# Kernel tuning notes

Hardware: AMD Instinct MI355X
Metric: run time of the kernel (lower is better)

## Reference

```python
import jax, jax.numpy as jnp
import numpy as np

DIM = 768
NUM_HEADS = 12
HEAD_DIM = DIM // NUM_HEADS
SCALE = HEAD_DIM ** -0.5


def setup_inputs() -> dict:
    key = jax.random.key(0)
    k1, k2, k3, k4 = jax.random.split(key, 4)
    B, N, C = 4, 2048, DIM
    x = jax.random.normal(k1, (B, N, C), dtype=jnp.float32)
    # nn.Linear(dim, 3*dim, bias=False): weight shape (3C, C), y = x @ W^T
    w_qkv = jax.random.normal(k2, (3 * C, C), dtype=jnp.float32) * (C ** -0.5)
    # nn.Linear(dim, dim) with default bias=True
    w_proj = jax.random.normal(k3, (C, C), dtype=jnp.float32) * (C ** -0.5)
    b_proj = jax.random.normal(k4, (C,), dtype=jnp.float32) * 0.02
    return {"x": x, "w_qkv": w_qkv, "w_proj": w_proj, "b_proj": b_proj}


def reference(x, w_qkv, w_proj, b_proj):
    B, N, C = x.shape
    H, D = NUM_HEADS, HEAD_DIM
    qkv = jnp.einsum('bnc,oc->bno', x, w_qkv)  # (B, N, 3C)
    qkv = qkv.reshape(B, N, 3, H, D).transpose(2, 0, 3, 1, 4)  # (3, B, H, N, D)
    q, k, v = qkv[0], qkv[1], qkv[2]
    attn = jnp.einsum('bhnd,bhmd->bhnm', q, k) * jnp.float32(SCALE)  # (B,H,N,N)
    attn = jax.nn.softmax(attn, axis=-1)
    out = jnp.einsum('bhnm,bhmd->bhnd', attn, v)  # (B,H,N,D)
    out = out.transpose(0, 2, 1, 3).reshape(B, N, C)
    out = jnp.einsum('bnc,oc->bno', out, w_proj) + b_proj
    return out
```

## Files before the change

kernel.cpp:

```cpp
#include <hip/hip_runtime.h>
#include <math.h>

#define B_ 4
#define N_ 2048
#define C_ 768
#define H_ 12
#define D_ 64
#define QKSCALE_ 0.18033688011112042f

typedef unsigned short u16;
typedef unsigned int u32;
typedef short s16x8 __attribute__((ext_vector_type(8)));
typedef float f32x4 __attribute__((ext_vector_type(4)));
typedef float f32x16 __attribute__((ext_vector_type(16)));

__device__ __forceinline__ u16 f2bf(float f) {
    union { float f; u32 u; } v; v.f = f;
    u32 r = (v.u + 0x7fffu + ((v.u >> 16) & 1u)) >> 16;
    return (u16)r;
}

__device__ __forceinline__ void gl_lds16(const u16* g, u16* l) {
    __builtin_amdgcn_global_load_lds(
        (__attribute__((address_space(1))) void*)g,
        (__attribute__((address_space(3))) void*)l, 16, 0, 0);
}

#define NX4_  (B_ * N_ * C_ / 4)
#define NWQ4_ (3 * C_ * C_ / 4)
#define NWP4_ (C_ * C_ / 4)
__global__ __launch_bounds__(256) void cvt_all(const float4* __restrict__ x,
                                               const float4* __restrict__ wq,
                                               const float4* __restrict__ wp,
                                               ushort4* __restrict__ xb,
                                               ushort4* __restrict__ wqb,
                                               ushort4* __restrict__ wpb)
{
    const int tot = NX4_ + NWQ4_ + NWP4_;
    int i = blockIdx.x * blockDim.x + threadIdx.x;
    const int stride = gridDim.x * blockDim.x;
    for (; i < tot; i += stride) {
        const float4* s; ushort4* d; int j;
        if (i < NX4_)              { s = x;  d = xb;  j = i; }
        else if (i < NX4_ + NWQ4_) { s = wq; d = wqb; j = i - NX4_; }
        else                       { s = wp; d = wpb; j = i - NX4_ - NWQ4_; }
        float4 v = s[j];
        ushort4 o;
        o.x = f2bf(v.x); o.y = f2bf(v.y); o.z = f2bf(v.z); o.w = f2bf(v.w);
        d[j] = o;
    }
}

template<int BM, int WPEU, bool OUT_BF16, bool BIAS, bool QSCALE>
__global__ __launch_bounds__(256, WPEU) void gemm_mfma(const u16* __restrict__ A,
                                                       const u16* __restrict__ Bm,
                                                       const float* __restrict__ bias,
                                                       void* __restrict__ Cout,
                                                       int M, int N, int K)
{
    constexpr int MF  = BM / 64;
    constexpr int AC  = BM / 32;
    constexpr int ASZ = BM * 64, BSZ = 128 * 64;
    __shared__ __align__(16) u16 As[2 * ASZ];
    __shared__ __align__(16) u16 Bs[2 * BSZ];
    const int tid  = threadIdx.x;
    const int wv   = tid >> 6;
    const int lane = tid & 63;
    const int l31  = lane & 31;
    const int hi   = lane >> 5;
    const int wm   = (wv >> 1) * (BM / 2);
    const int wn   = (wv & 1) * 64;

    const int gx   = gridDim.x;
    const int nwg  = gx * gridDim.y;
    const int wgid = blockIdx.y * gx + blockIdx.x;
    const int nid  = (wgid & 7) * (nwg >> 3) + (wgid >> 3);
    const int row0 = (nid / gx) * BM, col0 = (nid % gx) * 128;

    f32x16 acc[MF][2];
    #pragma unroll
    for (int i = 0; i < MF; i++)
        #pragma unroll
        for (int j = 0; j < 2; j++)
            #pragma unroll
            for (int r = 0; r < 16; r++) acc[i][j][r] = 0.f;

    const int srow   = lane >> 3;
    const int schunk = ((lane & 7) ^ srow) * 8;

    const int arow_base = (BM / 4) * wv;
    const u16* gA = A + (size_t)(row0 + arow_base + srow) * K + schunk;
    const u16* gB = Bm + (size_t)(col0 + 32 * wv + srow) * K + schunk;
    const int aoff = arow_base * 64;
    const int boff = (32 * wv) * 64;

    const int nIter = K / 64;

    #pragma unroll
    for (int c = 0; c < AC; c++)
        gl_lds16(gA + (size_t)(8 * c) * K, As + aoff + c * 8 * 64);
    #pragma unroll
    for (int c = 0; c < 4; c++)
        gl_lds16(gB + (size_t)(8 * c) * K, Bs + boff + c * 8 * 64);

    for (int t = 0; t < nIter; t++) {
        const int cur = t & 1;
        __syncthreads();
        if (t + 1 < nIter) {
            const int k1 = (t + 1) * 64;
            const int nb = cur ^ 1;
            #pragma unroll
            for (int c = 0; c < AC; c++)
                gl_lds16(gA + (size_t)(8 * c) * K + k1, As + nb * ASZ + aoff + c * 8 * 64);
            #pragma unroll
            for (int c = 0; c < 4; c++)
                gl_lds16(gB + (size_t)(8 * c) * K + k1, Bs + nb * BSZ + boff + c * 8 * 64);
        }
        const u16* __restrict__ Ac = As + cur * ASZ;
        const u16* __restrict__ Bc = Bs + cur * BSZ;
        #pragma unroll
        for (int kk = 0; kk < 4; kk++) {
            const int fo = ((2 * kk + hi) ^ (l31 & 7)) * 8;
            s16x8 af[MF], bfr[2];
            #pragma unroll
            for (int i = 0; i < MF; i++)
                af[i] = *(const s16x8*)&Ac[(wm + 32*i + l31) * 64 + fo];
            #pragma unroll
            for (int j = 0; j < 2; j++)
                bfr[j] = *(const s16x8*)&Bc[(wn + 32*j + l31) * 64 + fo];
            #pragma unroll
            for (int i = 0; i < MF; i++)
                #pragma unroll
                for (int j = 0; j < 2; j++)
                    acc[i][j] = __builtin_amdgcn_mfma_f32_32x32x16_bf16(af[i], bfr[j], acc[i][j], 0, 0, 0);
        }
    }

    #pragma unroll
    for (int i = 0; i < MF; i++) {
        #pragma unroll
        for (int j = 0; j < 2; j++) {
            const int col = col0 + wn + 32*j + l31;
            float bv = BIAS ? bias[col] : 0.f;
            #pragma unroll
            for (int r = 0; r < 16; r++) {
                const int row = row0 + wm + 32*i + (r & 3) + 8*(r >> 2) + 4*hi;
                float v = acc[i][j][r] + bv;
                if (QSCALE && col < C_) v *= QKSCALE_;
                if (OUT_BF16) ((u16*)Cout)[(size_t)row * N + col] = f2bf(v);
                else          ((float*)Cout)[(size_t)row * N + col] = v;
            }
        }
    }
}

__global__ __launch_bounds__(256, 3) void attn_mfma(const u16* __restrict__ qkv,
                                                    u16* __restrict__ attout)
{
    __shared__ __align__(16) u16 Ks[2][64 * 64];
    __shared__ __align__(16) u16 Vt[2][64][72];

    const int tid  = threadIdx.x;
    const int wv   = tid >> 6;
    const int lane = tid & 63;
    const int l31  = lane & 31;
    const int hi   = lane >> 5;

    const int wgid = blockIdx.y * gridDim.x + blockIdx.x;
    const int ix   = wgid >> 3;
    const int bh   = (wgid & 7) * 6 + (ix >> 4);
    const int n0   = (ix & 15) * 128;
    const int b = bh / H_, h = bh % H_;
    const size_t rs = 3 * C_;

    const u16* Qg = qkv + ((size_t)b * N_ + n0) * rs + h * D_;
    const u16* Kg = qkv + ((size_t)b * N_) * rs + C_ + h * D_;
    const u16* Vg = Kg + C_;

    s16x8 qf[4];
    #pragma unroll
    for (int kk = 0; kk < 4; kk++)
        qf[kk] = *(const s16x8*)(Qg + (size_t)(32*wv + l31) * rs + kk*16 + hi*8);

    const f32x16 z16 = {0.f,0.f,0.f,0.f,0.f,0.f,0.f,0.f,
                        0.f,0.f,0.f,0.f,0.f,0.f,0.f,0.f};
    f32x16 oacc[2] = {z16, z16};
    float li = 0.f;

    const int kkey = lane >> 3;
    const u16* Kg_l = Kg + (size_t)(16*wv + kkey) * rs + ((lane & 7) ^ kkey) * 8;

    const int vc = tid & 7, vp = tid >> 3;
    const int vkey0 = 2 * vp, vd0 = vc * 8;
    const int vcol0 = (vkey0 + 8 * vc) & 63;

    gl_lds16(Kg_l,                    &Ks[0][(16*wv) * 64]);
    gl_lds16(Kg_l + (size_t)8 * rs,   &Ks[0][(16*wv + 8) * 64]);

    s16x8 vr0, vr1;
    {
        const u16* vp2 = Vg + (size_t)vkey0 * rs + vd0;
        vr0 = *(const s16x8*)vp2; vr1 = *(const s16x8*)(vp2 + rs);
    }
    #pragma unroll
    for (int u = 0; u < 8; u++) {
        u32 pk = (u32)(u16)vr0[u] | ((u32)(u16)vr1[u] << 16);
        *(u32*)&Vt[0][vd0 + u][vcol0] = pk;
    }
    {
        const u16* vp2 = Vg + (size_t)(64 + vkey0) * rs + vd0;
        vr0 = *(const s16x8*)vp2; vr1 = *(const s16x8*)(vp2 + rs);
    }

    const int NT = N_ / 64;
    for (int t = 0; t < NT; t++) {
        const int cur = t & 1, nxt = cur ^ 1;
        __syncthreads();
        if (t + 1 < NT) {
            const size_t ko = (size_t)(t + 1) * 64 * rs;
            gl_lds16(Kg_l + ko,                  &Ks[nxt][(16*wv) * 64]);
            gl_lds16(Kg_l + ko + (size_t)8 * rs, &Ks[nxt][(16*wv + 8) * 64]);
            #pragma unroll
            for (int u = 0; u < 8; u++) {
                u32 pk = (u32)(u16)vr0[u] | ((u32)(u16)vr1[u] << 16);
                *(u32*)&Vt[nxt][vd0 + u][vcol0] = pk;
            }
        }
        if (t + 2 < NT) {
            const u16* vp2 = Vg + (size_t)((t+2)*64 + vkey0) * rs + vd0;
            vr0 = *(const s16x8*)vp2; vr1 = *(const s16x8*)(vp2 + rs);
        }

        #define KF(j, kk) (*(const s16x8*)&Ks[cur][(32*(j) + l31) * 64 + \
                           ((2*(kk) + hi) ^ (l31 & 7)) * 8])
        f32x16 st0 = __builtin_amdgcn_mfma_f32_32x32x16_bf16(KF(0,0), qf[0], z16, 0, 0, 0);
        f32x16 st1 = __builtin_amdgcn_mfma_f32_32x32x16_bf16(KF(1,0), qf[0], z16, 0, 0, 0);
        #pragma unroll
        for (int kk = 1; kk < 4; kk++) {
            st0 = __builtin_amdgcn_mfma_f32_32x32x16_bf16(KF(0,kk), qf[kk], st0, 0, 0, 0);
            st1 = __builtin_amdgcn_mfma_f32_32x32x16_bf16(KF(1,kk), qf[kk], st1, 0, 0, 0);
        }
        #undef KF

        #pragma unroll
        for (int j = 0; j < 2; j++) {
            const f32x16 s = j ? st1 : st0;
            float p[16];
            #pragma unroll
            for (int r = 0; r < 16; r++) p[r] = __builtin_amdgcn_exp2f(s[r]);
            #pragma unroll
            for (int r = 0; r < 16; r += 4)
                li += (p[r] + p[r+1]) + (p[r+2] + p[r+3]);
            u32 w[4][2];
            #pragma unroll
            for (int m = 0; m < 4; m++) {
                asm("v_cvt_pk_bf16_f32 %0, %1, %2"
                    : "=v"(w[m][0]) : "v"(p[4*m+0]), "v"(p[4*m+1]));
                asm("v_cvt_pk_bf16_f32 %0, %1, %2"
                    : "=v"(w[m][1]) : "v"(p[4*m+2]), "v"(p[4*m+3]));
            }
            #pragma unroll
            for (int h2 = 0; h2 < 2; h2++) {
                asm("v_permlane32_swap_b32 %0, %1"
                    : "+v"(w[2*h2][0]), "+v"(w[2*h2+1][0]));
                asm("v_permlane32_swap_b32 %0, %1"
                    : "+v"(w[2*h2][1]), "+v"(w[2*h2+1][1]));
                const int sp = 2*j + h2;
                union { u32 uw[4]; s16x8 v; } pa;
                pa.uw[0] = w[2*h2][0];   pa.uw[1] = w[2*h2][1];
                pa.uw[2] = w[2*h2+1][0]; pa.uw[3] = w[2*h2+1][1];
                #pragma unroll
                for (int j2 = 0; j2 < 2; j2++) {
                    const int pb = (2*sp + hi + 4*j2 + (l31 >> 3)) & 7;
                    s16x8 vb = *(const s16x8*)&Vt[cur][32*j2 + l31][pb * 8];
                    oacc[j2] = __builtin_amdgcn_mfma_f32_32x32x16_bf16(pa.v, vb, oacc[j2], 0, 0, 0);
                }
            }
        }
    }

    li += __shfl_xor(li, 32);
    const float inv = 1.f / li;
    #pragma unroll
    for (int r = 0; r < 16; r++) {
        const int qr = (r & 3) + 8 * (r >> 2) + 4 * hi;
        const float iv = __shfl(inv, qr);
        const size_t grow = (size_t)(b * N_ + n0 + 32*wv + qr);
        #pragma unroll
        for (int j2 = 0; j2 < 2; j2++)
            attout[grow * C_ + h * D_ + 32*j2 + l31] = f2bf(oacc[j2][r] * iv);
    }
}

extern "C" void kernel_launch(void* const* d_in, const int* in_sizes, int n_in,
                              void* d_out, int out_size, void* d_ws, size_t ws_size,
                              hipStream_t stream) {
    const float* x      = (const float*)d_in[0];
    const float* w_qkv  = (const float*)d_in[1];
    const float* w_proj = (const float*)d_in[2];
    const float* b_proj = (const float*)d_in[3];
    float* out = (float*)d_out;

    const int NX   = B_ * N_ * C_;
    const int NWQ  = 3 * C_ * C_;
    const int NWP  = C_ * C_;
    const int NQKV = B_ * N_ * 3 * C_;

    u16* xb   = (u16*)d_ws;
    u16* wqb  = xb + NX;
    u16* wpb  = wqb + NWQ;
    u16* qkvb = wpb + NWP;
    u16* attb = qkvb + NQKV;

    dim3 blk(256);

    cvt_all<<<768, blk, 0, stream>>>((const float4*)x, (const float4*)w_qkv,
                                     (const float4*)w_proj,
                                     (ushort4*)xb, (ushort4*)wqb, (ushort4*)wpb);

    const int M = B_ * N_;
    gemm_mfma<128, 2, true, false, true><<<dim3((3*C_)/128, M/128), blk, 0, stream>>>(
        xb, wqb, nullptr, qkvb, M, 3*C_, C_);

    attn_mfma<<<dim3(N_/128, B_ * H_), blk, 0, stream>>>(qkvb, attb);

    gemm_mfma<64, 3, false, true, false><<<dim3(C_/128, M/64), blk, 0, stream>>>(
        attb, wpb, b_proj, out, M, C_, C_);
}
```

Baseline: 207.8 us.

## Software-pipeline QK^T one tile ahead of softmax-PV with triple-buffered V

Restructures the attention loop so the QK^T MFMAs for tile t are issued after the softmax and PV of tile t-1, letting exp/convert VALU work overlap MFMA latency. V tiles in LDS are triple-buffered so the tile being consumed stays valid while the next one is written. The row-sum accumulation switches to packed v_pk_add_f32 and the V transpose uses byte permutes. The trade-off is more LDS and more live registers, which could lower occupancy.

```diff
diff --git a/kernel.cpp b/kernel.cpp
--- a/kernel.cpp
+++ b/kernel.cpp
@@ -11,6 +11,7 @@
 typedef unsigned short u16;
 typedef unsigned int u32;
 typedef short s16x8 __attribute__((ext_vector_type(8)));
+typedef float f32x2 __attribute__((ext_vector_type(2)));
 typedef float f32x4 __attribute__((ext_vector_type(4)));
 typedef float f32x16 __attribute__((ext_vector_type(16)));
 
@@ -158,7 +159,7 @@
                                                     u16* __restrict__ attout)
 {
     __shared__ __align__(16) u16 Ks[2][64 * 64];
-    __shared__ __align__(16) u16 Vt[2][64][72];
+    __shared__ __align__(16) u16 Vt[3][64][72];
 
     const int tid  = threadIdx.x;
     const int wv   = tid >> 6;
@@ -185,7 +186,7 @@
     const f32x16 z16 = {0.f,0.f,0.f,0.f,0.f,0.f,0.f,0.f,
                         0.f,0.f,0.f,0.f,0.f,0.f,0.f,0.f};
     f32x16 oacc[2] = {z16, z16};
-    float li = 0.f;
+    f32x2 li2 = {0.f, 0.f};
 
     const int kkey = lane >> 3;
     const u16* Kg_l = Kg + (size_t)(16*wv + kkey) * rs + ((lane & 7) ^ kkey) * 8;
@@ -194,70 +195,50 @@
     const int vkey0 = 2 * vp, vd0 = vc * 8;
     const int vcol0 = (vkey0 + 8 * vc) & 63;
 
-    gl_lds16(Kg_l,                    &Ks[0][(16*wv) * 64]);
-    gl_lds16(Kg_l + (size_t)8 * rs,   &Ks[0][(16*wv + 8) * 64]);
-
-    s16x8 vr0, vr1;
-    {
-        const u16* vp2 = Vg + (size_t)vkey0 * rs + vd0;
-        vr0 = *(const s16x8*)vp2; vr1 = *(const s16x8*)(vp2 + rs);
-    }
-    #pragma unroll
-    for (int u = 0; u < 8; u++) {
-        u32 pk = (u32)(u16)vr0[u] | ((u32)(u16)vr1[u] << 16);
-        *(u32*)&Vt[0][vd0 + u][vcol0] = pk;
-    }
-    {
-        const u16* vp2 = Vg + (size_t)(64 + vkey0) * rs + vd0;
-        vr0 = *(const s16x8*)vp2; vr1 = *(const s16x8*)(vp2 + rs);
-    }
-
-    const int NT = N_ / 64;
-    for (int t = 0; t < NT; t++) {
-        const int cur = t & 1, nxt = cur ^ 1;
-        __syncthreads();
-        if (t + 1 < NT) {
-            const size_t ko = (size_t)(t + 1) * 64 * rs;
-            gl_lds16(Kg_l + ko,                  &Ks[nxt][(16*wv) * 64]);
-            gl_lds16(Kg_l + ko + (size_t)8 * rs, &Ks[nxt][(16*wv + 8) * 64]);
-            #pragma unroll
-            for (int u = 0; u < 8; u++) {
-                u32 pk = (u32)(u16)vr0[u] | ((u32)(u16)vr1[u] << 16);
-                *(u32*)&Vt[nxt][vd0 + u][vcol0] = pk;
-            }
-        }
-        if (t + 2 < NT) {
-            const u16* vp2 = Vg + (size_t)((t+2)*64 + vkey0) * rs + vd0;
-            vr0 = *(const s16x8*)vp2; vr1 = *(const s16x8*)(vp2 + rs);
-        }
-
+    auto vstore = [&](int slot, const s16x8& va, const s16x8& vb2) {
+        union { s16x8 v; u32 d[4]; } u0, u1; u0.v = va; u1.v = vb2;
+        #pragma unroll
+        for (int i = 0; i < 4; i++) {
+            *(u32*)&Vt[slot][vd0 + 2*i    ][vcol0] =
+                __builtin_amdgcn_perm(u1.d[i], u0.d[i], 0x05040100u);
+            *(u32*)&Vt[slot][vd0 + 2*i + 1][vcol0] =
+                __builtin_amdgcn_perm(u1.d[i], u0.d[i], 0x07060302u);
+        }
+    };
+
+    auto qk = [&](int cur, f32x16& s0o, f32x16& s1o) {
         #define KF(j, kk) (*(const s16x8*)&Ks[cur][(32*(j) + l31) * 64 + \
                            ((2*(kk) + hi) ^ (l31 & 7)) * 8])
-        f32x16 st0 = __builtin_amdgcn_mfma_f32_32x32x16_bf16(KF(0,0), qf[0], z16, 0, 0, 0);
-        f32x16 st1 = __builtin_amdgcn_mfma_f32_32x32x16_bf16(KF(1,0), qf[0], z16, 0, 0, 0);
+        s0o = __builtin_amdgcn_mfma_f32_32x32x16_bf16(KF(0,0), qf[0], z16, 0, 0, 0);
+        s1o = __builtin_amdgcn_mfma_f32_32x32x16_bf16(KF(1,0), qf[0], z16, 0, 0, 0);
         #pragma unroll
         for (int kk = 1; kk < 4; kk++) {
-            st0 = __builtin_amdgcn_mfma_f32_32x32x16_bf16(KF(0,kk), qf[kk], st0, 0, 0, 0);
-            st1 = __builtin_amdgcn_mfma_f32_32x32x16_bf16(KF(1,kk), qf[kk], st1, 0, 0, 0);
+            s0o = __builtin_amdgcn_mfma_f32_32x32x16_bf16(KF(0,kk), qf[kk], s0o, 0, 0, 0);
+            s1o = __builtin_amdgcn_mfma_f32_32x32x16_bf16(KF(1,kk), qf[kk], s1o, 0, 0, 0);
         }
         #undef KF
-
+    };
+
+    auto softmax_pv = [&](const f32x16& s0v, const f32x16& s1v, int slot) {
         #pragma unroll
         for (int j = 0; j < 2; j++) {
-            const f32x16 s = j ? st1 : st0;
-            float p[16];
-            #pragma unroll
-            for (int r = 0; r < 16; r++) p[r] = __builtin_amdgcn_exp2f(s[r]);
-            #pragma unroll
-            for (int r = 0; r < 16; r += 4)
-                li += (p[r] + p[r+1]) + (p[r+2] + p[r+3]);
+            const f32x16 s = j ? s1v : s0v;
+            f32x2 pr[8];
+            #pragma unroll
+            for (int r = 0; r < 8; r++) {
+                pr[r].x = __builtin_amdgcn_exp2f(s[2*r]);
+                pr[r].y = __builtin_amdgcn_exp2f(s[2*r+1]);
+            }
+            #pragma unroll
+            for (int r = 0; r < 8; r++)
+                asm("v_pk_add_f32 %0, %0, %1" : "+v"(li2) : "v"(pr[r]));
             u32 w[4][2];
             #pragma unroll
             for (int m = 0; m < 4; m++) {
                 asm("v_cvt_pk_bf16_f32 %0, %1, %2"
-                    : "=v"(w[m][0]) : "v"(p[4*m+0]), "v"(p[4*m+1]));
+                    : "=v"(w[m][0]) : "v"(pr[2*m].x), "v"(pr[2*m].y));
                 asm("v_cvt_pk_bf16_f32 %0, %1, %2"
-                    : "=v"(w[m][1]) : "v"(p[4*m+2]), "v"(p[4*m+3]));
+                    : "=v"(w[m][1]) : "v"(pr[2*m+1].x), "v"(pr[2*m+1].y));
             }
             #pragma unroll
             for (int h2 = 0; h2 < 2; h2++) {
@@ -272,13 +253,61 @@
                 #pragma unroll
                 for (int j2 = 0; j2 < 2; j2++) {
                     const int pb = (2*sp + hi + 4*j2 + (l31 >> 3)) & 7;
-                    s16x8 vb = *(const s16x8*)&Vt[cur][32*j2 + l31][pb * 8];
+                    s16x8 vb = *(const s16x8*)&Vt[slot][32*j2 + l31][pb * 8];
                     oacc[j2] = __builtin_amdgcn_mfma_f32_32x32x16_bf16(pa.v, vb, oacc[j2], 0, 0, 0);
                 }
             }
         }
-    }
-
+    };
+
+    gl_lds16(Kg_l,                    &Ks[0][(16*wv) * 64]);
+    gl_lds16(Kg_l + (size_t)8 * rs,   &Ks[0][(16*wv + 8) * 64]);
+    s16x8 vr0, vr1;
+    {
+        const u16* vp2 = Vg + (size_t)vkey0 * rs + vd0;
+        vr0 = *(const s16x8*)vp2; vr1 = *(const s16x8*)(vp2 + rs);
+    }
+    vstore(0, vr0, vr1);
+    {
+        const u16* vp2 = Vg + (size_t)(64 + vkey0) * rs + vd0;
+        vr0 = *(const s16x8*)vp2; vr1 = *(const s16x8*)(vp2 + rs);
+    }
+
+    const int NT = N_ / 64;
+    f32x16 sp0, sp1;
+
+    __syncthreads();
+    {
+        const size_t ko = (size_t)64 * rs;
+        gl_lds16(Kg_l + ko,                  &Ks[1][(16*wv) * 64]);
+        gl_lds16(Kg_l + ko + (size_t)8 * rs, &Ks[1][(16*wv + 8) * 64]);
+        vstore(1, vr0, vr1);
+        const u16* vp2 = Vg + (size_t)(2*64 + vkey0) * rs + vd0;
+        vr0 = *(const s16x8*)vp2; vr1 = *(const s16x8*)(vp2 + rs);
+    }
+    qk(0, sp0, sp1);
+
+    int vwr = 2, vrd = 0;
+    for (int t = 1; t < NT; t++) {
+        __syncthreads();
+        if (t + 1 < NT) {
+            const size_t ko = (size_t)(t + 1) * 64 * rs;
+            gl_lds16(Kg_l + ko,                  &Ks[(t+1)&1][(16*wv) * 64]);
+            gl_lds16(Kg_l + ko + (size_t)8 * rs, &Ks[(t+1)&1][(16*wv + 8) * 64]);
+            vstore(vwr, vr0, vr1);
+        }
+        if (t + 2 < NT) {
+            const u16* vp2 = Vg + (size_t)((t+2)*64 + vkey0) * rs + vd0;
+            vr0 = *(const s16x8*)vp2; vr1 = *(const s16x8*)(vp2 + rs);
+        }
+        softmax_pv(sp0, sp1, vrd);
+        qk(t & 1, sp0, sp1);
+        vwr = (vwr == 2) ? 0 : vwr + 1;
+        vrd = (vrd == 2) ? 0 : vrd + 1;
+    }
+    softmax_pv(sp0, sp1, vrd);
+
+    float li = li2.x + li2.y;
     li += __shfl_xor(li, 32);
     const float inv = 1.f / li;
     #pragma unroll
```

Measured after the change: 207.3 us. No clear change (-0.3%).
